# Kernel optimization log

Hardware: AMD Instinct MI355X
Metric: run time of the kernel (lower is better)

## Reference

```python
import jax, jax.numpy as jnp
import numpy as np

N, OBS, H, M, L = 512, 32, 128, 128, 3


def _w(key, shape, fan_in):
    return jax.random.normal(key, shape, dtype=jnp.float32) / np.sqrt(fan_in)


def setup_inputs() -> dict:
    key = jax.random.key(0)
    ks = iter(jax.random.split(key, 64))
    inp = {}
    inp["obs"] = jax.random.normal(next(ks), (N, OBS), dtype=jnp.float32)
    inp["pos"] = jax.random.uniform(next(ks), (N, 2), dtype=jnp.float32)
    # encoder: obs_dim -> H -> H -> H
    inp["enc_W1"] = _w(next(ks), (H, OBS), OBS); inp["enc_b1"] = jnp.zeros((H,), jnp.float32)
    inp["enc_W2"] = _w(next(ks), (H, H), H);     inp["enc_b2"] = jnp.zeros((H,), jnp.float32)
    inp["enc_W3"] = _w(next(ks), (H, H), H);     inp["enc_b3"] = jnp.zeros((H,), jnp.float32)
    # per-layer message MLPs: (2H+1) -> M -> M -> M, stacked over L layers
    inp["msg_W1"] = _w(next(ks), (L, M, 2 * H + 1), 2 * H + 1); inp["msg_b1"] = jnp.zeros((L, M), jnp.float32)
    inp["msg_W2"] = _w(next(ks), (L, M, M), M);                 inp["msg_b2"] = jnp.zeros((L, M), jnp.float32)
    inp["msg_W3"] = _w(next(ks), (L, M, M), M);                 inp["msg_b3"] = jnp.zeros((L, M), jnp.float32)
    # per-layer update MLPs: (H+M) -> H -> H -> H, stacked over L layers
    inp["upd_W1"] = _w(next(ks), (L, H, H + M), H + M); inp["upd_b1"] = jnp.zeros((L, H), jnp.float32)
    inp["upd_W2"] = _w(next(ks), (L, H, H), H);         inp["upd_b2"] = jnp.zeros((L, H), jnp.float32)
    inp["upd_W3"] = _w(next(ks), (L, H, H), H);         inp["upd_b3"] = jnp.zeros((L, H), jnp.float32)
    return inp


def _mlp3(x, W1, b1, W2, b2, W3, b3):
    h = jax.nn.relu(x @ W1.T + b1)
    h = jax.nn.relu(h @ W2.T + b2)
    return h @ W3.T + b3


def reference(obs, pos, enc_W1, enc_b1, enc_W2, enc_b2, enc_W3, enc_b3,
              msg_W1, msg_b1, msg_W2, msg_b2, msg_W3, msg_b3,
              upd_W1, upd_b1, upd_W2, upd_b2, upd_W3, upd_b3):
    n = obs.shape[0]
    h = enc_W1.shape[0]
    z = _mlp3(obs, enc_W1, enc_b1, enc_W2, enc_b2, enc_W3, enc_b3)  # (N, H)
    # pairwise distances; guard diagonal sqrt(0) for grad safety, then zero it
    diff = pos[:, None, :] - pos[None, :, :]                  # (N, N, 2)
    sq = jnp.sum(diff * diff, axis=-1)                        # (N, N)
    eye = jnp.eye(n, dtype=pos.dtype)
    dist = jnp.sqrt(jnp.where(eye > 0, 1.0, sq)) * (1.0 - eye)
    nondiag = (1.0 - eye)[:, :, None]
    n_layers = msg_W1.shape[0]
    for l in range(n_layers):
        W1 = msg_W1[l]
        Wi, Wj, wd = W1[:, :h], W1[:, h:2 * h], W1[:, 2 * h]  # split concat [z_i, z_j, d]
        A = z @ Wi.T                                          # (N, M) receiver term
        B = z @ Wj.T                                          # (N, M) sender term
        h1 = jax.nn.relu(A[:, None, :] + B[None, :, :] + dist[:, :, None] * wd + msg_b1[l])  # (N, N, M)
        h2 = jax.nn.relu(jnp.einsum('ijm,km->ijk', h1, msg_W2[l]) + msg_b2[l])
        m = jnp.einsum('ijm,km->ijk', h2, msg_W3[l]) + msg_b3[l]
        m = m * nondiag                                       # exclude j == i
        msum = jnp.sum(m, axis=1)                             # (N, M) sum over senders j
        z = _mlp3(jnp.concatenate([z, msum], axis=-1),
                  upd_W1[l], upd_b1[l], upd_W2[l], upd_b2[l], upd_W3[l], upd_b3[l])
    return z
```

## Files before the change

### kernel.cpp

```cpp
#include <hip/hip_runtime.h>

#define NA 512
#define NOBS 32
#define NH 128

typedef const float* fp32p;
typedef __attribute__((ext_vector_type(8))) short bf16x8;
typedef __attribute__((ext_vector_type(4))) float f32x4;

__device__ __forceinline__ unsigned cvt_pk_bf16(float lo, float hi) {
    unsigned r;
    asm("v_cvt_pk_bf16_f32 %0, %1, %2" : "=v"(r) : "v"(lo), "v"(hi));
    return r;
}

__device__ __forceinline__ bf16x8 wfrag_f4(const float* p) {
    float4 u = *(const float4*)p;
    float4 v = *(const float4*)(p + 4);
    union { unsigned w[4]; bf16x8 f; } r;
    r.w[0] = cvt_pk_bf16(u.x, u.y);
    r.w[1] = cvt_pk_bf16(u.z, u.w);
    r.w[2] = cvt_pk_bf16(v.x, v.y);
    r.w[3] = cvt_pk_bf16(v.z, v.w);
    return r.f;
}

#define HSTR 136

__global__ __launch_bounds__(512) void enc_ab_kernel(
    fp32p obs, fp32p eW1, fp32p eb1, fp32p eW2, fp32p eb2, fp32p eW3, fp32p eb3,
    fp32p mW1, float* __restrict__ z, float* __restrict__ A, float* __restrict__ B) {
    const int i = blockIdx.x;
    const int t = threadIdx.x;
    const int nn = t >> 2;
    const int ks = t & 3;

    __shared__ float xs0[NOBS];
    __shared__ float part[4 * NH];
    __shared__ float part2[4 * NH];
    __shared__ float hx[NH], hy[NH], zz[NH];

    if (t < NOBS) xs0[t] = obs[(size_t)i * NOBS + t];
    __syncthreads();
    {
        const float* wr = eW1 + (size_t)nn * NOBS + ks * 8;
        const float4 w0 = *(const float4*)wr;
        const float4 w1 = *(const float4*)(wr + 4);
        const float4 x0 = *(const float4*)&xs0[ks * 8];
        const float4 x1 = *(const float4*)&xs0[ks * 8 + 4];
        part[ks * NH + nn] = w0.x * x0.x + w0.y * x0.y + w0.z * x0.z + w0.w * x0.w +
                             w1.x * x1.x + w1.y * x1.y + w1.z * x1.z + w1.w * x1.w;
    }
    __syncthreads();
    if (t < NH)
        hx[t] = fmaxf(eb1[t] + part[t] + part[NH + t] + part[2 * NH + t] + part[3 * NH + t], 0.f);
    __syncthreads();
    {
        const float* wr = eW2 + (size_t)nn * NH + ks * 4;
        float p = 0.f;
        #pragma unroll
        for (int it = 0; it < 8; ++it) {
            const float4 wv = *(const float4*)(wr + it * 16);
            const float4 xv = *(const float4*)&hx[it * 16 + ks * 4];
            p += wv.x * xv.x + wv.y * xv.y + wv.z * xv.z + wv.w * xv.w;
        }
        part[ks * NH + nn] = p;
    }
    __syncthreads();
    if (t < NH)
        hy[t] = fmaxf(eb2[t] + part[t] + part[NH + t] + part[2 * NH + t] + part[3 * NH + t], 0.f);
    __syncthreads();
    {
        const float* wr = eW3 + (size_t)nn * NH + ks * 4;
        float p = 0.f;
        #pragma unroll
        for (int it = 0; it < 8; ++it) {
            const float4 wv = *(const float4*)(wr + it * 16);
            const float4 xv = *(const float4*)&hy[it * 16 + ks * 4];
            p += wv.x * xv.x + wv.y * xv.y + wv.z * xv.z + wv.w * xv.w;
        }
        part[ks * NH + nn] = p;
    }
    __syncthreads();
    if (t < NH) {
        const float v = eb3[t] + part[t] + part[NH + t] + part[2 * NH + t] + part[3 * NH + t];
        z[(size_t)i * NH + t] = v;
        zz[t] = v;
    }
    __syncthreads();
    {
        const float* pr = mW1 + (size_t)nn * 257;
        float pa = 0.f, pb = 0.f;
        #pragma unroll
        for (int it = 0; it < 8; ++it) {
            #pragma unroll
            for (int j = 0; j < 4; ++j) {
                const int k = it * 16 + ks * 4 + j;
                const float x = zz[k];
                pa += x * pr[k];
                pb += x * pr[NH + k];
            }
        }
        part[ks * NH + nn] = pa;
        part2[ks * NH + nn] = pb;
    }
    __syncthreads();
    if (t < NH) {
        A[(size_t)i * NH + t] = part[t] + part[NH + t] + part[2 * NH + t] + part[3 * NH + t];
        B[(size_t)i * NH + t] = part2[t] + part2[NH + t] + part2[2 * NH + t] + part2[3 * NH + t];
    }
}

__global__ __launch_bounds__(512) void msg_upd_kernel(
    const float* __restrict__ A, const float* __restrict__ B,
    fp32p pos, const float* __restrict__ zin,
    fp32p W1l, fp32p b1, fp32p W2, fp32p b2, fp32p W3, fp32p b3,
    fp32p uW1, fp32p ub1, fp32p uW2, fp32p ub2, fp32p uW3, fp32p ub3,
    fp32p msgW1n, int do_ab,
    float* __restrict__ zout, float* __restrict__ An, float* __restrict__ Bn) {
    const int i = blockIdx.x;
    const int t = threadIdx.x;
    const int lane = t & 63;
    const int w = t >> 6;
    const int q = lane >> 4;
    const int c = lane & 15;
    const int ncol = w * 16 + c;

    __shared__ short h1s[128 * HSTR];
    __shared__ short h2s[128 * HSTR];
    __shared__ float distrow[NA];
    __shared__ float amrow[NH];
    __shared__ float wdsr[NH];
    __shared__ float xs2[2 * NH];
    __shared__ float part[4 * NH];
    __shared__ float part2[4 * NH];
    __shared__ float hx[NH], hy[NH], hz[NH];

    if (t < NH) {
        amrow[t] = A[i * NH + t] + b1[t];
        wdsr[t]  = W1l[t * 257 + 256];
        xs2[t] = zin[(size_t)i * NH + t];
    }
    {
        const float2 pi = *(const float2*)&pos[2 * i];
        const float2 pj = *(const float2*)&pos[2 * t];
        const float dx = pi.x - pj.x, dy = pi.y - pj.y;
        const float s = dx * dx + dy * dy;
        distrow[t] = (t == i) ? 0.0f : sqrtf(s);
    }

    bf16x8 w2f[4], w3f[4];
    {
        const float* w2r = W2 + (size_t)ncol * NH + q * 8;
        const float* w3r = W3 + (size_t)ncol * NH + q * 8;
        #pragma unroll
        for (int kb = 0; kb < 4; ++kb) {
            w2f[kb] = wfrag_f4(w2r + kb * 32);
            w3f[kb] = wfrag_f4(w3r + kb * 32);
        }
    }
    const float b2n = b2[ncol];

    const int m2 = lane * 2;
    float psum = 0.0f;

    for (int c4 = 0; c4 < 4; ++c4) {
        const int j0 = c4 * 128;
        __syncthreads();

        {
            const float am0 = amrow[m2],     am1 = amrow[m2 + 1];
            const float wd0 = wdsr[m2],      wd1 = wdsr[m2 + 1];
            #pragma unroll
            for (int rr = 0; rr < 16; ++rr) {
                const int row = rr * 8 + w;
                const int jg  = j0 + row;
                const float2 bv = *(const float2*)&B[(size_t)jg * NH + m2];
                const float d = distrow[jg];
                const float v0 = fmaxf(fmaf(d, wd0, am0 + bv.x), 0.0f);
                const float v1 = fmaxf(fmaf(d, wd1, am1 + bv.y), 0.0f);
                *(unsigned*)&h1s[row * HSTR + m2] = cvt_pk_bf16(v0, v1);
            }
        }
        __syncthreads();

        #pragma unroll
        for (int jt = 0; jt < 8; ++jt) {
            f32x4 acc = {0.f, 0.f, 0.f, 0.f};
            const short* arow = &h1s[(jt * 16 + c) * HSTR + q * 8];
            #pragma unroll
            for (int kb = 0; kb < 4; ++kb) {
                bf16x8 a = *(const bf16x8*)(arow + kb * 32);
                acc = __builtin_amdgcn_mfma_f32_16x16x32_bf16(a, w2f[kb], acc, 0, 0, 0);
            }
            const int orow = jt * 16 + q * 4;
            const unsigned p01 = cvt_pk_bf16(fmaxf(acc[0] + b2n, 0.0f),
                                             fmaxf(acc[1] + b2n, 0.0f));
            const unsigned p23 = cvt_pk_bf16(fmaxf(acc[2] + b2n, 0.0f),
                                             fmaxf(acc[3] + b2n, 0.0f));
            h2s[(orow + 0) * HSTR + ncol] = (short)p01;
            h2s[(orow + 1) * HSTR + ncol] = (short)(p01 >> 16);
            h2s[(orow + 2) * HSTR + ncol] = (short)p23;
            h2s[(orow + 3) * HSTR + ncol] = (short)(p23 >> 16);
        }
        __syncthreads();

        #pragma unroll
        for (int jt = 0; jt < 8; ++jt) {
            f32x4 acc = {0.f, 0.f, 0.f, 0.f};
            const short* arow = &h2s[(jt * 16 + c) * HSTR + q * 8];
            #pragma unroll
            for (int kb = 0; kb < 4; ++kb) {
                bf16x8 a = *(const bf16x8*)(arow + kb * 32);
                acc = __builtin_amdgcn_mfma_f32_16x16x32_bf16(a, w3f[kb], acc, 0, 0, 0);
            }
            #pragma unroll
            for (int r = 0; r < 4; ++r) {
                const int jg = j0 + jt * 16 + q * 4 + r;
                if (jg != i) psum += acc[r];
            }
        }
    }

    psum += __shfl_xor(psum, 16, 64);
    psum += __shfl_xor(psum, 32, 64);
    if (lane < 16) xs2[NH + ncol] = psum + 511.0f * b3[ncol];
    __syncthreads();

    const int nn = t >> 2;
    const int ks = t & 3;
    {
        const float* wr = uW1 + (size_t)nn * 256 + ks * 4;
        float p = 0.f;
        #pragma unroll
        for (int it = 0; it < 16; ++it) {
            const float4 wv = *(const float4*)(wr + it * 16);
            const float4 xv = *(const float4*)&xs2[it * 16 + ks * 4];
            p += wv.x * xv.x + wv.y * xv.y + wv.z * xv.z + wv.w * xv.w;
        }
        part[ks * NH + nn] = p;
    }
    __syncthreads();
    if (t < NH)
        hx[t] = fmaxf(ub1[t] + part[t] + part[NH + t] + part[2 * NH + t] + part[3 * NH + t], 0.f);
    __syncthreads();
    {
        const float* wr = uW2 + (size_t)nn * NH + ks * 4;
        float p = 0.f;
        #pragma unroll
        for (int it = 0; it < 8; ++it) {
            const float4 wv = *(const float4*)(wr + it * 16);
            const float4 xv = *(const float4*)&hx[it * 16 + ks * 4];
            p += wv.x * xv.x + wv.y * xv.y + wv.z * xv.z + wv.w * xv.w;
        }
        part[ks * NH + nn] = p;
    }
    __syncthreads();
    if (t < NH)
        hy[t] = fmaxf(ub2[t] + part[t] + part[NH + t] + part[2 * NH + t] + part[3 * NH + t], 0.f);
    __syncthreads();
    {
        const float* wr = uW3 + (size_t)nn * NH + ks * 4;
        float p = 0.f;
        #pragma unroll
        for (int it = 0; it < 8; ++it) {
            const float4 wv = *(const float4*)(wr + it * 16);
            const float4 xv = *(const float4*)&hy[it * 16 + ks * 4];
            p += wv.x * xv.x + wv.y * xv.y + wv.z * xv.z + wv.w * xv.w;
        }
        part[ks * NH + nn] = p;
    }
    __syncthreads();
    if (t < NH) {
        const float v = ub3[t] + part[t] + part[NH + t] + part[2 * NH + t] + part[3 * NH + t];
        zout[(size_t)i * NH + t] = v;
        hz[t] = v;
    }
    if (!do_ab) return;
    __syncthreads();
    {
        const float* pr = msgW1n + (size_t)nn * 257;
        float pa = 0.f, pb = 0.f;
        #pragma unroll
        for (int it = 0; it < 8; ++it) {
            #pragma unroll
            for (int j = 0; j < 4; ++j) {
                const int k = it * 16 + ks * 4 + j;
                const float x = hz[k];
                pa += x * pr[k];
                pb += x * pr[NH + k];
            }
        }
        part[ks * NH + nn] = pa;
        part2[ks * NH + nn] = pb;
    }
    __syncthreads();
    if (t < NH) {
        An[(size_t)i * NH + t] = part[t] + part[NH + t] + part[2 * NH + t] + part[3 * NH + t];
        Bn[(size_t)i * NH + t] = part2[t] + part2[NH + t] + part2[2 * NH + t] + part2[3 * NH + t];
    }
}

extern "C" void kernel_launch(void* const* d_in, const int* in_sizes, int n_in,
                              void* d_out, int out_size, void* d_ws, size_t ws_size,
                              hipStream_t stream) {
    fp32p obs   = (fp32p)d_in[0];
    fp32p pos   = (fp32p)d_in[1];
    fp32p encW1 = (fp32p)d_in[2];  fp32p encb1 = (fp32p)d_in[3];
    fp32p encW2 = (fp32p)d_in[4];  fp32p encb2 = (fp32p)d_in[5];
    fp32p encW3 = (fp32p)d_in[6];  fp32p encb3 = (fp32p)d_in[7];
    fp32p msgW1 = (fp32p)d_in[8];  fp32p msgb1 = (fp32p)d_in[9];
    fp32p msgW2 = (fp32p)d_in[10]; fp32p msgb2 = (fp32p)d_in[11];
    fp32p msgW3 = (fp32p)d_in[12]; fp32p msgb3 = (fp32p)d_in[13];
    fp32p updW1 = (fp32p)d_in[14]; fp32p updb1 = (fp32p)d_in[15];
    fp32p updW2 = (fp32p)d_in[16]; fp32p updb2 = (fp32p)d_in[17];
    fp32p updW3 = (fp32p)d_in[18]; fp32p updb3 = (fp32p)d_in[19];

    float* ws = (float*)d_ws;
    float* zA = ws;
    float* zB = zA + NA * NH;
    float* A0 = zB + NA * NH;
    float* B0 = A0 + NA * NH;
    float* A1 = B0 + NA * NH;
    float* B1 = A1 + NA * NH;

    enc_ab_kernel<<<NA, 512, 0, stream>>>(obs, encW1, encb1, encW2, encb2,
                                          encW3, encb3, msgW1, zA, A0, B0);

    float* zin = zA;  float* zout = zB;
    float* Ac = A0;   float* Bc = B0;
    float* An = A1;   float* Bn = B1;
    for (int l = 0; l < 3; ++l) {
        const int do_ab = (l < 2);
        float* dst = (l == 2) ? (float*)d_out : zout;
        msg_upd_kernel<<<NA, 512, 0, stream>>>(Ac, Bc, pos, zin,
            msgW1 + (size_t)l * 128 * 257, msgb1 + l * 128,
            msgW2 + (size_t)l * 128 * 128, msgb2 + l * 128,
            msgW3 + (size_t)l * 128 * 128, msgb3 + l * 128,
            updW1 + (size_t)l * 256 * 128, updb1 + l * 128,
            updW2 + (size_t)l * 128 * 128, updb2 + l * 128,
            updW3 + (size_t)l * 128 * 128, updb3 + l * 128,
            msgW1 + (size_t)(l + 1 < 3 ? l + 1 : 0) * 128 * 257, do_ab,
            dst, An, Bn);
        float* tmp;
        tmp = zin; zin = zout; zout = tmp;
        tmp = Ac; Ac = An; An = tmp;
        tmp = Bc; Bc = Bn; Bn = tmp;
    }
}
```

Measured before the change: 219.3 us.

## Fuse message layer-2 and layer-3 GEMMs in registers, dropping h2 shared buffer

The second message GEMM is computed transposed so each wave's output fragment feeds straight into a K=16 MFMA for the third layer. That layer accumulates over senders in registers per wave, so the h2 shared-memory round trip and one block barrier per chunk are gone. Cross-wave partial sums are reduced at the end through a shared buffer. The diagonal sender is masked by zeroing its bf16 activations. Launch bounds now request two blocks per CU, which trades register pressure (eight accumulator tiles plus W3 fragments) for occupancy and uses more, smaller MFMAs.

```diff
diff --git a/kernel.cpp b/kernel.cpp
--- a/kernel.cpp
+++ b/kernel.cpp
@@ -6,6 +6,7 @@
 
 typedef const float* fp32p;
 typedef __attribute__((ext_vector_type(8))) short bf16x8;
+typedef __attribute__((ext_vector_type(4))) short bf16x4;
 typedef __attribute__((ext_vector_type(4))) float f32x4;
 
 __device__ __forceinline__ unsigned cvt_pk_bf16(float lo, float hi) {
@@ -25,6 +26,21 @@
     return r.f;
 }
 
+#if __has_builtin(__builtin_amdgcn_mfma_f32_16x16x16bf16_1k)
+#define MFMA_K16(A, B, C) __builtin_amdgcn_mfma_f32_16x16x16bf16_1k(A, B, C, 0, 0, 0)
+#elif __has_builtin(__builtin_amdgcn_mfma_f32_16x16x16_bf16)
+#define MFMA_K16(A, B, C) __builtin_amdgcn_mfma_f32_16x16x16_bf16(A, B, C, 0, 0, 0)
+#else
+__device__ __forceinline__ f32x4 mfma_k16_asm(bf16x4 a, bf16x4 b, f32x4 c) {
+    f32x4 d;
+    asm volatile("v_mfma_f32_16x16x16_bf16 %0, %1, %2, %3\n\t"
+                 "s_nop 7\n\ts_nop 7\n\ts_nop 7"
+                 : "=v"(d) : "v"(a), "v"(b), "v"(c));
+    return d;
+}
+#define MFMA_K16(A, B, C) mfma_k16_asm(A, B, C)
+#endif
+
 #define HSTR 136
 
 __global__ __launch_bounds__(512) void enc_ab_kernel(
@@ -111,7 +127,7 @@
     }
 }
 
-__global__ __launch_bounds__(512) void msg_upd_kernel(
+__global__ __launch_bounds__(512, 2) void msg_upd_kernel(
     const float* __restrict__ A, const float* __restrict__ B,
     fp32p pos, const float* __restrict__ zin,
     fp32p W1l, fp32p b1, fp32p W2, fp32p b2, fp32p W3, fp32p b3,
@@ -127,13 +143,13 @@
     const int ncol = w * 16 + c;
 
     __shared__ short h1s[128 * HSTR];
-    __shared__ short h2s[128 * HSTR];
     __shared__ float distrow[NA];
     __shared__ float amrow[NH];
     __shared__ float wdsr[NH];
     __shared__ float xs2[2 * NH];
     __shared__ float part[4 * NH];
     __shared__ float part2[4 * NH];
+    __shared__ float partsum[8 * NH];
     __shared__ float hx[NH], hy[NH], hz[NH];
 
     if (t < NH) {
@@ -149,20 +165,28 @@
         distrow[t] = (t == i) ? 0.0f : sqrtf(s);
     }
 
-    bf16x8 w2f[4], w3f[4];
+    bf16x8 w2f[4];
     {
         const float* w2r = W2 + (size_t)ncol * NH + q * 8;
-        const float* w3r = W3 + (size_t)ncol * NH + q * 8;
-        #pragma unroll
-        for (int kb = 0; kb < 4; ++kb) {
-            w2f[kb] = wfrag_f4(w2r + kb * 32);
-            w3f[kb] = wfrag_f4(w3r + kb * 32);
-        }
-    }
-    const float b2n = b2[ncol];
+        #pragma unroll
+        for (int kb = 0; kb < 4; ++kb) w2f[kb] = wfrag_f4(w2r + kb * 32);
+    }
+    bf16x4 w3s[8];
+    #pragma unroll
+    for (int n2t = 0; n2t < 8; ++n2t) {
+        const float4 wv = *(const float4*)(W3 + (size_t)(n2t * 16 + c) * NH + w * 16 + q * 4);
+        union { unsigned u[2]; bf16x4 v; } r;
+        r.u[0] = cvt_pk_bf16(wv.x, wv.y);
+        r.u[1] = cvt_pk_bf16(wv.z, wv.w);
+        w3s[n2t] = r.v;
+    }
+    const float4 b2q = *(const float4*)(b2 + w * 16 + q * 4);
+
+    f32x4 acc2[8];
+    #pragma unroll
+    for (int n2t = 0; n2t < 8; ++n2t) acc2[n2t] = (f32x4){0.f, 0.f, 0.f, 0.f};
 
     const int m2 = lane * 2;
-    float psum = 0.0f;
 
     for (int c4 = 0; c4 < 4; ++c4) {
         const int j0 = c4 * 128;
@@ -186,45 +210,47 @@
 
         #pragma unroll
         for (int jt = 0; jt < 8; ++jt) {
-            f32x4 acc = {0.f, 0.f, 0.f, 0.f};
+            f32x4 acc1 = {0.f, 0.f, 0.f, 0.f};
             const short* arow = &h1s[(jt * 16 + c) * HSTR + q * 8];
             #pragma unroll
             for (int kb = 0; kb < 4; ++kb) {
                 bf16x8 a = *(const bf16x8*)(arow + kb * 32);
-                acc = __builtin_amdgcn_mfma_f32_16x16x32_bf16(a, w2f[kb], acc, 0, 0, 0);
+                acc1 = __builtin_amdgcn_mfma_f32_16x16x32_bf16(w2f[kb], a, acc1, 0, 0, 0);
             }
-            const int orow = jt * 16 + q * 4;
-            const unsigned p01 = cvt_pk_bf16(fmaxf(acc[0] + b2n, 0.0f),
-                                             fmaxf(acc[1] + b2n, 0.0f));
-            const unsigned p23 = cvt_pk_bf16(fmaxf(acc[2] + b2n, 0.0f),
-                                             fmaxf(acc[3] + b2n, 0.0f));
-            h2s[(orow + 0) * HSTR + ncol] = (short)p01;
-            h2s[(orow + 1) * HSTR + ncol] = (short)(p01 >> 16);
-            h2s[(orow + 2) * HSTR + ncol] = (short)p23;
-            h2s[(orow + 3) * HSTR + ncol] = (short)(p23 >> 16);
-        }
-        __syncthreads();
-
-        #pragma unroll
-        for (int jt = 0; jt < 8; ++jt) {
-            f32x4 acc = {0.f, 0.f, 0.f, 0.f};
-            const short* arow = &h2s[(jt * 16 + c) * HSTR + q * 8];
-            #pragma unroll
-            for (int kb = 0; kb < 4; ++kb) {
-                bf16x8 a = *(const bf16x8*)(arow + kb * 32);
-                acc = __builtin_amdgcn_mfma_f32_16x16x32_bf16(a, w3f[kb], acc, 0, 0, 0);
-            }
-            #pragma unroll
-            for (int r = 0; r < 4; ++r) {
-                const int jg = j0 + jt * 16 + q * 4 + r;
-                if (jg != i) psum += acc[r];
-            }
-        }
-    }
-
-    psum += __shfl_xor(psum, 16, 64);
-    psum += __shfl_xor(psum, 32, 64);
-    if (lane < 16) xs2[NH + ncol] = psum + 511.0f * b3[ncol];
+            const float v0 = fmaxf(acc1[0] + b2q.x, 0.f);
+            const float v1 = fmaxf(acc1[1] + b2q.y, 0.f);
+            const float v2 = fmaxf(acc1[2] + b2q.z, 0.f);
+            const float v3 = fmaxf(acc1[3] + b2q.w, 0.f);
+            unsigned u0 = cvt_pk_bf16(v0, v1);
+            unsigned u1 = cvt_pk_bf16(v2, v3);
+            if (j0 + jt * 16 + c == i) { u0 = 0u; u1 = 0u; }
+            union { unsigned u[2]; bf16x4 v; } bf;
+            bf.u[0] = u0; bf.u[1] = u1;
+            #pragma unroll
+            for (int n2t = 0; n2t < 8; ++n2t)
+                acc2[n2t] = MFMA_K16(w3s[n2t], bf.v, acc2[n2t]);
+        }
+    }
+
+    #pragma unroll
+    for (int n2t = 0; n2t < 8; ++n2t) {
+        #pragma unroll
+        for (int r = 0; r < 4; ++r) {
+            float v = acc2[n2t][r];
+            v += __shfl_xor(v, 1, 64);
+            v += __shfl_xor(v, 2, 64);
+            v += __shfl_xor(v, 4, 64);
+            v += __shfl_xor(v, 8, 64);
+            if (c == 0) partsum[w * NH + n2t * 16 + q * 4 + r] = v;
+        }
+    }
+    __syncthreads();
+    if (t < NH) {
+        float s = 0.f;
+        #pragma unroll
+        for (int ww = 0; ww < 8; ++ww) s += partsum[ww * NH + t];
+        xs2[NH + t] = s + 511.0f * b3[t];
+    }
     __syncthreads();
 
     const int nn = t >> 2;
```

New measurement: 238.4 us. +8.7%, slower.

## Software-pipeline h1 build with second GEMM across sender chunks

Applied to the files above, without the earlier changes.

Restructures the per-chunk loop so the h1 tile for the next sender chunk is built while the second MFMA GEMM for the current chunk runs, cutting one barrier per iteration. The build writes h1s while GEMM2 reads h2s, so the buffers do not conflict. The loop-invariant am/wd loads are hoisted out of the loop. This trades some extra register pressure for more overlap between VALU/global loads and MFMA work.

```diff
diff --git a/kernel.cpp b/kernel.cpp
--- a/kernel.cpp
+++ b/kernel.cpp
@@ -164,63 +164,82 @@
     const int m2 = lane * 2;
     float psum = 0.0f;
 
+    __syncthreads();
+    const float am0 = amrow[m2], am1 = amrow[m2 + 1];
+    const float wd0 = wdsr[m2],  wd1 = wdsr[m2 + 1];
+
+#define BUILD(c4_) do {                                                      \
+        const int j0_ = (c4_) * 128;                                         \
+        _Pragma("unroll")                                                    \
+        for (int rr = 0; rr < 16; ++rr) {                                    \
+            const int row_ = rr * 8 + w;                                     \
+            const int jg_ = j0_ + row_;                                      \
+            const float2 bv_ = *(const float2*)&B[(size_t)jg_ * NH + m2];    \
+            const float d_ = distrow[jg_];                                   \
+            const float v0_ = fmaxf(fmaf(d_, wd0, am0 + bv_.x), 0.0f);       \
+            const float v1_ = fmaxf(fmaf(d_, wd1, am1 + bv_.y), 0.0f);       \
+            *(unsigned*)&h1s[row_ * HSTR + m2] = cvt_pk_bf16(v0_, v1_);      \
+        }                                                                    \
+    } while (0)
+
+#define GEMM1() do {                                                         \
+        _Pragma("unroll")                                                    \
+        for (int jt = 0; jt < 8; ++jt) {                                     \
+            f32x4 acc = {0.f, 0.f, 0.f, 0.f};                                \
+            const short* arow = &h1s[(jt * 16 + c) * HSTR + q * 8];          \
+            _Pragma("unroll")                                                \
+            for (int kb = 0; kb < 4; ++kb) {                                 \
+                bf16x8 a = *(const bf16x8*)(arow + kb * 32);                 \
+                acc = __builtin_amdgcn_mfma_f32_16x16x32_bf16(a, w2f[kb], acc, 0, 0, 0); \
+            }                                                                \
+            const int orow = jt * 16 + q * 4;                                \
+            const unsigned p01 = cvt_pk_bf16(fmaxf(acc[0] + b2n, 0.0f),      \
+                                             fmaxf(acc[1] + b2n, 0.0f));     \
+            const unsigned p23 = cvt_pk_bf16(fmaxf(acc[2] + b2n, 0.0f),      \
+                                             fmaxf(acc[3] + b2n, 0.0f));     \
+            h2s[(orow + 0) * HSTR + ncol] = (short)p01;                      \
+            h2s[(orow + 1) * HSTR + ncol] = (short)(p01 >> 16);              \
+            h2s[(orow + 2) * HSTR + ncol] = (short)p23;                      \
+            h2s[(orow + 3) * HSTR + ncol] = (short)(p23 >> 16);              \
+        }                                                                    \
+    } while (0)
+
+#define GEMM2(c4_) do {                                                      \
+        const int j0_ = (c4_) * 128;                                         \
+        _Pragma("unroll")                                                    \
+        for (int jt = 0; jt < 8; ++jt) {                                     \
+            f32x4 acc = {0.f, 0.f, 0.f, 0.f};                                \
+            const short* arow = &h2s[(jt * 16 + c) * HSTR + q * 8];          \
+            _Pragma("unroll")                                                \
+            for (int kb = 0; kb < 4; ++kb) {                                 \
+                bf16x8 a = *(const bf16x8*)(arow + kb * 32);                 \
+                acc = __builtin_amdgcn_mfma_f32_16x16x32_bf16(a, w3f[kb], acc, 0, 0, 0); \
+            }                                                                \
+            _Pragma("unroll")                                                \
+            for (int r = 0; r < 4; ++r) {                                    \
+                const int jg_ = j0_ + jt * 16 + q * 4 + r;                   \
+                if (jg_ != i) psum += acc[r];                                \
+            }                                                                \
+        }                                                                    \
+    } while (0)
+
+    BUILD(0);
+    __syncthreads();
+    GEMM1();
     for (int c4 = 0; c4 < 4; ++c4) {
-        const int j0 = c4 * 128;
         __syncthreads();
-
-        {
-            const float am0 = amrow[m2],     am1 = amrow[m2 + 1];
-            const float wd0 = wdsr[m2],      wd1 = wdsr[m2 + 1];
-            #pragma unroll
-            for (int rr = 0; rr < 16; ++rr) {
-                const int row = rr * 8 + w;
-                const int jg  = j0 + row;
-                const float2 bv = *(const float2*)&B[(size_t)jg * NH + m2];
-                const float d = distrow[jg];
-                const float v0 = fmaxf(fmaf(d, wd0, am0 + bv.x), 0.0f);
-                const float v1 = fmaxf(fmaf(d, wd1, am1 + bv.y), 0.0f);
-                *(unsigned*)&h1s[row * HSTR + m2] = cvt_pk_bf16(v0, v1);
-            }
-        }
-        __syncthreads();
-
-        #pragma unroll
-        for (int jt = 0; jt < 8; ++jt) {
-            f32x4 acc = {0.f, 0.f, 0.f, 0.f};
-            const short* arow = &h1s[(jt * 16 + c) * HSTR + q * 8];
-            #pragma unroll
-            for (int kb = 0; kb < 4; ++kb) {
-                bf16x8 a = *(const bf16x8*)(arow + kb * 32);
-                acc = __builtin_amdgcn_mfma_f32_16x16x32_bf16(a, w2f[kb], acc, 0, 0, 0);
-            }
-            const int orow = jt * 16 + q * 4;
-            const unsigned p01 = cvt_pk_bf16(fmaxf(acc[0] + b2n, 0.0f),
-                                             fmaxf(acc[1] + b2n, 0.0f));
-            const unsigned p23 = cvt_pk_bf16(fmaxf(acc[2] + b2n, 0.0f),
-                                             fmaxf(acc[3] + b2n, 0.0f));
-            h2s[(orow + 0) * HSTR + ncol] = (short)p01;
-            h2s[(orow + 1) * HSTR + ncol] = (short)(p01 >> 16);
-            h2s[(orow + 2) * HSTR + ncol] = (short)p23;
-            h2s[(orow + 3) * HSTR + ncol] = (short)(p23 >> 16);
-        }
-        __syncthreads();
-
-        #pragma unroll
-        for (int jt = 0; jt < 8; ++jt) {
-            f32x4 acc = {0.f, 0.f, 0.f, 0.f};
-            const short* arow = &h2s[(jt * 16 + c) * HSTR + q * 8];
-            #pragma unroll
-            for (int kb = 0; kb < 4; ++kb) {
-                bf16x8 a = *(const bf16x8*)(arow + kb * 32);
-                acc = __builtin_amdgcn_mfma_f32_16x16x32_bf16(a, w3f[kb], acc, 0, 0, 0);
-            }
-            #pragma unroll
-            for (int r = 0; r < 4; ++r) {
-                const int jg = j0 + jt * 16 + q * 4 + r;
-                if (jg != i) psum += acc[r];
-            }
-        }
-    }
+        if (c4 < 3) {
+            BUILD(c4 + 1);
+            GEMM2(c4);
+            __syncthreads();
+            GEMM1();
+        } else {
+            GEMM2(c4);
+        }
+    }
+#undef BUILD
+#undef GEMM1
+#undef GEMM2
 
     psum += __shfl_xor(psum, 16, 64);
     psum += __shfl_xor(psum, 32, 64);
```

New measurement: 209.6 us. 4.4% less time.
